# Kernel tuning notes

Hardware: AMD Instinct MI355X
Metric: run time of the kernel (lower is better)

## Reference

```python
import jax, jax.numpy as jnp
import numpy as np
from jax import lax

EPS = 1e-5

def setup_inputs() -> dict:
    key = jax.random.key(0)
    ks = jax.random.split(key, 8)
    B, D, H, W = 2, 96, 96, 96
    K, N, R = 4, 16, 6
    return {
        "x": jax.random.normal(ks[0], (B, D, H, W), jnp.float32),
        "x_proj_weight": jax.random.normal(ks[1], (K, R + 2 * N, D), jnp.float32) * 0.05,
        "dt_projs_weight": jax.random.normal(ks[2], (K, D, R), jnp.float32) * 0.05,
        "dt_projs_bias": jax.random.normal(ks[3], (K, D), jnp.float32) * 0.05,
        "A_logs": jax.random.uniform(ks[4], (K * D, N), jnp.float32, 0.0, 1.0),
        "Ds": jax.random.normal(ks[5], (K * D,), jnp.float32) * 0.1,
        "norm_weight": jnp.ones((D,), jnp.float32),
        "norm_bias": jnp.zeros((D,), jnp.float32),
    }

def _cross_scan(x):
    # x: [B,C,H,W] -> xs: [B,4,C,L]; dirs: row-major, col-major, and their flips
    B, C, H, W = x.shape
    x_hw = x.reshape(B, C, H * W)
    x_wh = jnp.swapaxes(x, 2, 3).reshape(B, C, H * W)
    return jnp.stack([x_hw, x_wh, x_hw[..., ::-1], x_wh[..., ::-1]], axis=1)

def _cross_merge(ys, H, W):
    # ys: [B,4,C,L] -> y: [B,C,L]
    B, K, C, L = ys.shape
    ys = ys[:, 0:2] + ys[:, 2:4][..., ::-1]
    y_wh = jnp.swapaxes(ys[:, 1].reshape(B, C, W, H), 2, 3).reshape(B, C, L)
    return ys[:, 0] + y_wh

def _forward(x, x_proj_weight, dt_projs_weight, dt_projs_bias, A_logs, Ds,
             norm_weight, norm_bias):
    B, D, H, W = x.shape
    L = H * W
    K, _, R = dt_projs_weight.shape
    N = A_logs.shape[1]

    xs = _cross_scan(x)                                        # [B,K,D,L]
    x_dbl = jnp.einsum('bkdl,kcd->bkcl', xs, x_proj_weight)    # [B,K,R+2N,L]
    dts, Bs, Cs = x_dbl[:, :, :R], x_dbl[:, :, R:R + N], x_dbl[:, :, R + N:]
    dts = jnp.einsum('bkrl,kdr->bkdl', dts, dt_projs_weight)   # [B,K,D,L]

    A = -jnp.exp(A_logs).reshape(K, D, N)                      # [K,D,N]
    delta = jax.nn.softplus(dts + dt_projs_bias[None, :, :, None])  # [B,K,D,L]

    # time-major for scan
    u_t = jnp.moveaxis(xs, 3, 0)       # [L,B,K,D]
    d_t = jnp.moveaxis(delta, 3, 0)    # [L,B,K,D]
    B_t = jnp.moveaxis(Bs, 3, 0)       # [L,B,K,N]
    C_t = jnp.moveaxis(Cs, 3, 0)       # [L,B,K,N]

    def step(h, inp):
        u, dlt, b, c = inp
        h = jnp.exp(dlt[..., None] * A) * h + (dlt * u)[..., None] * b[:, :, None, :]
        y = jnp.einsum('bkdn,bkn->bkd', h, c)
        return h, y

    h0 = jnp.zeros((B, K, D, N), xs.dtype)
    _, ys = lax.scan(step, h0, (u_t, d_t, B_t, C_t))           # ys: [L,B,K,D]
    ys = jnp.moveaxis(ys, 0, 3)                                # [B,K,D,L]
    ys = ys + Ds.reshape(1, K, D, 1) * xs                      # skip term

    y = _cross_merge(ys, H, W)                                 # [B,D,L]
    y = jnp.swapaxes(y, 1, 2)                                  # [B,L,D]
    # out_norm: LayerNorm over channel dim
    mu = y.mean(-1, keepdims=True)
    var = y.var(-1, keepdims=True)
    y = (y - mu) / jnp.sqrt(var + EPS) * norm_weight + norm_bias
    return y.reshape(B, H, W, D)

def reference(x, x_proj_weight, dt_projs_weight, dt_projs_bias, A_logs, Ds,
              norm_weight, norm_bias):
    return _forward(x, x_proj_weight, dt_projs_weight, dt_projs_bias,
                    A_logs, Ds, norm_weight, norm_bias)
```

## Files before the change

kernel.cpp:

```cpp
#include <hip/hip_runtime.h>
#include <hip/hip_bf16.h>
#include <hip/hip_fp16.h>


constexpr int Bn = 2, Kn = 4, Dn = 96, Hn = 96, Wn = 96, Ln = Hn * Wn;
constexpr int Nn = 16, Rn = 6;
constexpr int TLn = 36, CCn = 256, CLn = 36;

#define DI __device__ __forceinline__

typedef _Float16 half2v __attribute__((ext_vector_type(2)));

DI float bf2f(unsigned short u) { return __uint_as_float(((unsigned)u) << 16); }
DI bool probe_bf16(const void* nw) { return ((const unsigned*)nw)[0] == 0x3F803F80u; }
DI float ld_in(const void* p, long i, bool bf) {
  return bf ? bf2f(((const unsigned short*)p)[i]) : ((const float*)p)[i];
}
DI float fexp2(float x) {
#if __has_builtin(__builtin_amdgcn_exp2f)
  return __builtin_amdgcn_exp2f(x);
#else
  return exp2f(x);
#endif
}
DI float softplus_fast(float v) {
  return (v > 15.f) ? v : __logf(1.f + __expf(v));
}
DI float dot2acc(unsigned a, unsigned b, float c) {
#if __has_builtin(__builtin_amdgcn_fdot2)
  half2v av, bv;
  __builtin_memcpy(&av, &a, 4);
  __builtin_memcpy(&bv, &b, 4);
  return __builtin_amdgcn_fdot2(av, bv, c, false);
#else
  __half2 ah = *(__half2*)&a, bh = *(__half2*)&b;
  float2 af = __half22float2(ah), bf2_ = __half22float2(bh);
  return fmaf(af.y, bf2_.y, fmaf(af.x, bf2_.x, c));
#endif
}
DI float quad_reduce_add(float v) {
  int a = __builtin_amdgcn_mov_dpp(__float_as_int(v), 0xB1, 0xF, 0xF, true);
  v += __int_as_float(a);
  int b = __builtin_amdgcn_mov_dpp(__float_as_int(v), 0x4E, 0xF, 0xF, true);
  v += __int_as_float(b);
  return v;
}
constexpr float LOG2E = 1.44269504088896340736f;

__global__ __launch_bounds__(256) void k_prep(
    const void* __restrict__ x, const void* __restrict__ xpw,
    const void* __restrict__ dtw, const void* __restrict__ dtb,
    const void* __restrict__ Al, const void* __restrict__ Ds,
    const void* __restrict__ nw, const void* __restrict__ nb,
    float* __restrict__ xl, float* __restrict__ xlT,
    __half* __restrict__ wp_h, unsigned* __restrict__ wdt_p,
    float* __restrict__ bias_f, float* __restrict__ Al_f,
    float* __restrict__ dsum, float* __restrict__ nw_f, float* __restrict__ nb_f) {
  __shared__ float tile[96 * 49];
  bool bf = probe_bf16(nw);
  int h = blockIdx.x, wh = blockIdx.y, b = blockIdx.z;
  int w0 = wh * 48;
  int tid = threadIdx.x;
  int fi = ((blockIdx.z * gridDim.y + blockIdx.y) * gridDim.x + blockIdx.x) *
               256 + tid;
  int fgs = gridDim.x * gridDim.y * gridDim.z * 256;
  for (int i = fi; i < Kn * 4000; i += fgs) {
    int k = i / 4000, r = i - k * 4000;
    int c = r / 100, dd = r - c * 100;
    wp_h[i] = __float2half(
        (c < 38 && dd < 96) ? ld_in(xpw, (long)k * 38 * 96 + c * 96 + dd, bf)
                            : 0.f);
  }
  for (int i = fi; i < Kn * Dn; i += fgs) {
    __half2 h01 = __floats2half2_rn(ld_in(dtw, (long)i * 6 + 0, bf),
                                    ld_in(dtw, (long)i * 6 + 1, bf));
    __half2 h23 = __floats2half2_rn(ld_in(dtw, (long)i * 6 + 2, bf),
                                    ld_in(dtw, (long)i * 6 + 3, bf));
    __half2 h45 = __floats2half2_rn(ld_in(dtw, (long)i * 6 + 4, bf),
                                    ld_in(dtw, (long)i * 6 + 5, bf));
    wdt_p[i * 3 + 0] = *(unsigned*)&h01;
    wdt_p[i * 3 + 1] = *(unsigned*)&h23;
    wdt_p[i * 3 + 2] = *(unsigned*)&h45;
    bias_f[i] = ld_in(dtb, i, bf);
  }
  for (int i = fi; i < Kn * Dn * Nn; i += fgs)
    Al_f[i] = -__expf(ld_in(Al, i, bf)) * LOG2E;
  for (int i = fi; i < Dn; i += fgs) {
    dsum[i] = ld_in(Ds, i, bf) + ld_in(Ds, 96 + i, bf) +
              ld_in(Ds, 192 + i, bf) + ld_in(Ds, 288 + i, bf);
    nw_f[i] = ld_in(nw, i, bf);
    nb_f[i] = ld_in(nb, i, bf);
  }
  long srcbase = (long)b * Dn * Ln + (long)h * 96 + w0;
  for (int i = tid; i < 96 * 48; i += 256) {
    int d = i / 48, w = i - d * 48;
    tile[d * 49 + w] = ld_in(x, srcbase + (long)d * Ln + w, bf);
  }
  __syncthreads();
  float* xlb = xl + (size_t)b * Ln * 96;
  float* xTb = xlT + (size_t)b * Ln * 96;
  for (int i = tid; i < 48 * 96; i += 256) {
    int w = i / 96, d = i - w * 96;
    float v = tile[d * 49 + w];
    xlb[(size_t)(h * 96 + w0 + w) * 96 + d] = v;
    xTb[(size_t)((w0 + w) * 96 + h) * 96 + d] = v;
  }
}

__global__ __launch_bounds__(256) void k_proj(
    const float* __restrict__ xl, const float* __restrict__ xlT,
    const __half* __restrict__ wp_h, const unsigned* __restrict__ wdt_p,
    const float* __restrict__ bias_f, const float* __restrict__ Al_f,
    __half2* __restrict__ ddu, __half* __restrict__ BCh,
    float* __restrict__ PSg) {
  constexpr int TL = TLn;
  __shared__ __half xt[TL * 102];
  __shared__ __half wp[40 * 100];
  __shared__ __half xd2[TL * 40];
  __shared__ unsigned wdt_u[96 * 4];
  __shared__ float bias[96];
  int tile = blockIdx.x, k = blockIdx.y, b = blockIdx.z;
  int l0 = tile * TL;
  int tid = threadIdx.x;
  bool rev = (k & 2) != 0;

  {
    const uint4* wsrc = (const uint4*)(wp_h + (size_t)k * 4000);
    for (int i = tid; i < 500; i += 256) ((uint4*)wp)[i] = wsrc[i];
    const unsigned* dsrc = wdt_p + (size_t)k * 288;
    for (int i = tid; i < 288; i += 256) {
      int d = i / 3, r = i - d * 3;
      wdt_u[d * 4 + r] = dsrc[i];
    }
    if (tid < 96) bias[tid] = bias_f[k * 96 + tid];
  }
  {
    const float* xsrc = ((k & 1) ? xlT : xl) + (size_t)b * Ln * 96;
    for (int i = tid; i < TL * 24; i += 256) {
      int r = i / 24, q = i - r * 24;
      int g = rev ? (Ln - 1 - l0 - r) : (l0 + r);
      float4 v = *(const float4*)(xsrc + (size_t)g * 96 + q * 4);
      *(__half2*)(&xt[r * 102 + q * 4]) = __floats2half2_rn(v.x, v.y);
      *(__half2*)(&xt[r * 102 + q * 4 + 2]) = __floats2half2_rn(v.z, v.w);
    }
  }
  __syncthreads();

  {
    for (int it = tid; it < TL * 8; it += 256) {
      int j = it >> 3, cg = it & 7;
      int c0 = cg * 5;
      float acc[5] = {0.f, 0.f, 0.f, 0.f, 0.f};
      for (int dd = 0; dd < 96; dd += 4) {
        uint2 xa = *(const uint2*)&xt[j * 102 + dd];
#pragma unroll
        for (int i = 0; i < 5; ++i) {
          uint2 wv = *(const uint2*)&wp[(c0 + i) * 100 + dd];
          acc[i] = dot2acc(xa.x, wv.x, acc[i]);
          acc[i] = dot2acc(xa.y, wv.y, acc[i]);
        }
      }
#pragma unroll
      for (int i = 0; i < 5; ++i) xd2[j * 40 + c0 + i] = __float2half(acc[i]);
    }
  }
  __syncthreads();

  size_t bk = (size_t)b * 4 + k;
  {
    __half2* o = (__half2*)(BCh + (bk * (size_t)Ln + l0) * 32);
    for (int i = tid; i < TL * 16; i += 256) {
      int j = i >> 4, cp = i & 15;
      int c = cp * 2;
      int ng = c >> 3, idx = c & 7;
      int ch = (idx < 4) ? (6 + ng * 4 + idx) : (22 + ng * 4 + (idx - 4));
      o[i] = *(const __half2*)&xd2[j * 40 + ch];
    }
  }
  if (tid < 192) {
    int d = tid >> 1, hg = tid & 1;
    unsigned wv0 = wdt_u[d * 4], wv1 = wdt_u[d * 4 + 1], wv2 = wdt_u[d * 4 + 2];
    float bd = bias[d];
    float ac2[8];
    *(float4*)&ac2[0] = *(const float4*)&Al_f[(k * 96 + d) * 16 + hg * 8];
    *(float4*)&ac2[4] = *(const float4*)&Al_f[(k * 96 + d) * 16 + hg * 8 + 4];
    float spsum = 0.f;
    float S[8] = {0.f, 0.f, 0.f, 0.f, 0.f, 0.f, 0.f, 0.f};
    __half2* dcol = ddu + (bk * (size_t)Ln + l0) * 96 + d;
#pragma unroll 2
    for (int t = 0; t < TL; ++t) {
      uint2 xr01 = *(const uint2*)&xd2[t * 40];
      unsigned xr2 = *(const unsigned*)&xd2[t * 40 + 4];
      float v = dot2acc(xr01.x, wv0,
                dot2acc(xr01.y, wv1,
                dot2acc(xr2, wv2, bd)));
      float sp = softplus_fast(v);
      __half sph = __float2half(sp);
      float spc = __half2float(sph);
      float u = __half2float(xt[t * 102 + d]);
      __half fyh = __float2half(spc * u);
      float fy = __half2float(fyh);
      if (hg == 0) dcol[(size_t)t * 96] = __halves2half2(sph, fyh);
      spsum += spc;
      unsigned bw0 = *(const unsigned*)&xd2[t * 40 + 6 + hg * 8];
      unsigned bw1 = *(const unsigned*)&xd2[t * 40 + 8 + hg * 8];
      unsigned bw2 = *(const unsigned*)&xd2[t * 40 + 10 + hg * 8];
      unsigned bw3 = *(const unsigned*)&xd2[t * 40 + 12 + hg * 8];
      unsigned bws[4] = {bw0, bw1, bw2, bw3};
#pragma unroll
      for (int w = 0; w < 4; ++w) {
        float2 Bv = __half22float2(*(__half2*)&bws[w]);
        float a0 = fexp2(spc * ac2[w * 2]);
        S[w * 2] = fmaf(a0, S[w * 2], fy * Bv.x);
        float a1 = fexp2(spc * ac2[w * 2 + 1]);
        S[w * 2 + 1] = fmaf(a1, S[w * 2 + 1], fy * Bv.y);
      }
    }
    float P[8];
#pragma unroll
    for (int j = 0; j < 8; ++j) P[j] = fexp2(spsum * ac2[j]);
    size_t ob = ((size_t)(bk * 96 + d) * CCn + tile) * 32 + hg * 8;
    *(float4*)&PSg[ob] = make_float4(P[0], P[1], P[2], P[3]);
    *(float4*)&PSg[ob + 4] = make_float4(P[4], P[5], P[6], P[7]);
    *(float4*)&PSg[ob + 16] = make_float4(S[0], S[1], S[2], S[3]);
    *(float4*)&PSg[ob + 20] = make_float4(S[4], S[5], S[6], S[7]);
  }
}

__global__ __launch_bounds__(256) void k_midscan(float* __restrict__ PSg) {
  __shared__ float Pl[256], Sl[256];
  int bkd = blockIdx.x;
  int tid = threadIdx.x;
  int g = tid >> 4, n = tid & 15;
  constexpr int CPG = CCn / 16;
  size_t base = ((size_t)bkd * CCn + (size_t)g * CPG) * 32 + n;
  float Pr[CPG], Sr[CPG];
#pragma unroll
  for (int i = 0; i < CPG; ++i) {
    Pr[i] = PSg[base + (size_t)i * 32];
    Sr[i] = PSg[base + (size_t)i * 32 + 16];
  }
  float Pa = 1.f, Sa = 0.f;
#pragma unroll
  for (int i = 0; i < CPG; ++i) { Sa = fmaf(Pr[i], Sa, Sr[i]); Pa *= Pr[i]; }
  Pl[tid] = Pa;
  Sl[tid] = Sa;
  __syncthreads();
#pragma unroll
  for (int s = 1; s < 16; s <<= 1) {
    float Pp = 1.f, Sp = 0.f;
    if (g >= s) { Pp = Pl[(g - s) * 16 + n]; Sp = Sl[(g - s) * 16 + n]; }
    __syncthreads();
    if (g >= s) {
      Sl[tid] = fmaf(Pl[tid], Sp, Sl[tid]);
      Pl[tid] *= Pp;
    }
    __syncthreads();
  }
  float h = (g == 0) ? 0.f : Sl[(g - 1) * 16 + n];
#pragma unroll
  for (int i = 0; i < CPG; ++i) {
    PSg[base + (size_t)i * 32] = h;
    h = fmaf(Pr[i], h, Sr[i]);
  }
}

__global__ __launch_bounds__(192) void k_scan2(
    const __half2* __restrict__ ddu, const __half* __restrict__ BCh,
    const float* __restrict__ Al_f, const float* __restrict__ PSg,
    __half* __restrict__ ysH) {
  __shared__ __half2 dd_s[CLn * 96];
  __shared__ __half bc_s[CLn * 32];
  int chunk = blockIdx.x, k = blockIdx.y, b = blockIdx.z;
  int tid = threadIdx.x;
  int dp = tid >> 2, ng = tid & 3;
  int d0 = dp * 2, n0 = ng * 4;
  int bk = b * 4 + k;
  int t0 = chunk * CLn;
  float ac[2][4];
#pragma unroll
  for (int dd = 0; dd < 2; ++dd)
#pragma unroll
    for (int j = 0; j < 4; ++j)
      ac[dd][j] = Al_f[(k * 96 + d0 + dd) * 16 + n0 + j];
  {
    const uint4* dsrc = (const uint4*)(ddu + ((size_t)bk * Ln + t0) * 96);
    uint4* ddst = (uint4*)dd_s;
    for (int i = tid; i < CLn * 96 / 4; i += 192) ddst[i] = dsrc[i];
    const uint4* bsrc = (const uint4*)(BCh + ((size_t)bk * Ln + t0) * 32);
    uint4* bdst = (uint4*)bc_s;
    for (int i = tid; i < CLn * 32 * 2 / 16; i += 192) bdst[i] = bsrc[i];
  }
  float4 ha = *(const float4*)(PSg + ((size_t)(bk * 96 + d0) * CCn + chunk) * 32 + n0);
  float4 hb = *(const float4*)(PSg + ((size_t)(bk * 96 + d0 + 1) * CCn + chunk) * 32 + n0);
  float h[2][4] = {{ha.x, ha.y, ha.z, ha.w}, {hb.x, hb.y, hb.z, hb.w}};
  __syncthreads();

#pragma unroll 2
  for (int t = 0; t < CLn; ++t) {
    union { uint2 u; __half2 h2[2]; } dv;
    dv.u = *(const uint2*)&dd_s[t * 96 + d0];
    union { uint4 u; __half2 h2[4]; } bc;
    bc.u = *(const uint4*)&bc_s[t * 32 + ng * 8];
    float2 f0 = __half22float2(dv.h2[0]);
    float2 f1 = __half22float2(dv.h2[1]);
    float2 b01 = __half22float2(bc.h2[0]);
    float2 b23 = __half22float2(bc.h2[1]);
    float2 c01 = __half22float2(bc.h2[2]);
    float2 c23 = __half22float2(bc.h2[3]);
    float Ba[4] = {b01.x, b01.y, b23.x, b23.y};
    float Ca[4] = {c01.x, c01.y, c23.x, c23.y};
    float py0 = 0.f, py1 = 0.f;
#pragma unroll
    for (int j = 0; j < 4; ++j) {
      float a0 = fexp2(f0.x * ac[0][j]);
      h[0][j] = fmaf(a0, h[0][j], f0.y * Ba[j]);
      py0 = fmaf(h[0][j], Ca[j], py0);
      float a1 = fexp2(f1.x * ac[1][j]);
      h[1][j] = fmaf(a1, h[1][j], f1.y * Ba[j]);
      py1 = fmaf(h[1][j], Ca[j], py1);
    }
    py0 = quad_reduce_add(py0);
    py1 = quad_reduce_add(py1);
    if (ng == 0)
      *(__half2*)&ysH[((size_t)bk * Ln + t0 + t) * 96 + d0] =
          __halves2half2(__float2half(py0), __float2half(py1));
  }
}

__global__ __launch_bounds__(256) void k_merge_ln(
    const __half* __restrict__ ysH, const float* __restrict__ xl,
    const float* __restrict__ dsum, const void* __restrict__ nwraw,
    const float* __restrict__ nw_f, const float* __restrict__ nb_f,
    void* __restrict__ outv) {
  __shared__ float yt[32 * 98];
  __shared__ float nwf[96], nbf[96], dsm[96], mu_s[32], rs_s[32];
  bool bf = probe_bf16(nwraw);
  int tile = blockIdx.x, b = blockIdx.y;
  int h0 = (tile / 12) * 4, w0 = (tile % 12) * 8;
  int tid = threadIdx.x;
  if (tid < 96) {
    nwf[tid] = nw_f[tid];
    nbf[tid] = nb_f[tid];
    dsm[tid] = dsum[tid];
  }
  const __half* y0 = ysH + (size_t)(b * 4 + 0) * Ln * 96;
  const __half* y1 = ysH + (size_t)(b * 4 + 1) * Ln * 96;
  const __half* y2 = ysH + (size_t)(b * 4 + 2) * Ln * 96;
  const __half* y3 = ysH + (size_t)(b * 4 + 3) * Ln * 96;
  const float* xb = xl + (size_t)b * Ln * 96;
  __syncthreads();
  for (int i = tid; i < 32 * 48; i += 256) {
    int rr = i / 48, dp = i - rr * 48, d = dp * 2;
    int hh = h0 + (rr >> 3), ww = w0 + (rr & 7);
    int l = hh * 96 + ww, t1 = ww * 96 + hh;
    float2 v0 = __half22float2(*(const __half2*)&y0[(size_t)l * 96 + d]);
    float2 v1 = __half22float2(*(const __half2*)&y1[(size_t)t1 * 96 + d]);
    float2 v2 = __half22float2(*(const __half2*)&y2[(size_t)(Ln - 1 - l) * 96 + d]);
    float2 v3 = __half22float2(*(const __half2*)&y3[(size_t)(Ln - 1 - t1) * 96 + d]);
    float2 xv = *(const float2*)&xb[(size_t)l * 96 + d];
    float2 r;
    r.x = v0.x + v1.x + v2.x + v3.x + dsm[d] * xv.x;
    r.y = v0.y + v1.y + v2.y + v3.y + dsm[d + 1] * xv.y;
    *(float2*)&yt[rr * 98 + d] = r;
  }
  __syncthreads();
  {
    int rr = tid >> 3, qq = tid & 7;
    float s = 0.f, ss = 0.f;
#pragma unroll 4
    for (int j = 0; j < 12; ++j) {
      float v = yt[rr * 98 + qq * 12 + j];
      s += v;
      ss += v * v;
    }
#pragma unroll
    for (int m = 1; m < 8; m <<= 1) {
      s += __shfl_xor(s, m, 64);
      ss += __shfl_xor(ss, m, 64);
    }
    if (qq == 0) {
      float mu = s * (1.f / 96.f);
      float var = fmaxf(ss * (1.f / 96.f) - mu * mu, 0.f);
      mu_s[rr] = mu;
      rs_s[rr] = rsqrtf(var + 1e-5f);
    }
  }
  __syncthreads();
  for (int i = tid; i < 32 * 48; i += 256) {
    int rr = i / 48, dp = i - rr * 48, d = dp * 2;
    int hh = h0 + (rr >> 3), ww = w0 + (rr & 7);
    size_t idx = ((size_t)b * Ln + hh * 96 + ww) * 96 + d;
    float2 yv = *(const float2*)&yt[rr * 98 + d];
    float mu = mu_s[rr], rs = rs_s[rr];
    float o0 = (yv.x - mu) * rs * nwf[d] + nbf[d];
    float o1 = (yv.y - mu) * rs * nwf[d + 1] + nbf[d + 1];
    if (bf) {
      union { unsigned u; unsigned short us[2]; } pk;
      __hip_bfloat16 b0 = __float2bfloat16(o0), b1 = __float2bfloat16(o1);
      pk.us[0] = *(unsigned short*)&b0;
      pk.us[1] = *(unsigned short*)&b1;
      *(unsigned*)&((__hip_bfloat16*)outv)[idx] = pk.u;
    } else {
      *(float2*)&((float*)outv)[idx] = make_float2(o0, o1);
    }
  }
}

extern "C" void kernel_launch(void* const* d_in, const int* in_sizes, int n_in,
                              void* d_out, int out_size, void* d_ws, size_t ws_size,
                              hipStream_t stream) {
  const void* x   = d_in[0];
  const void* xpw = d_in[1];
  const void* dtw = d_in[2];
  const void* dtb = d_in[3];
  const void* Al  = d_in[4];
  const void* Ds  = d_in[5];
  const void* nw  = d_in[6];
  const void* nb  = d_in[7];

  char* ws = (char*)d_ws;
  size_t off = 0;
  auto alloc = [&](size_t bytes) {
    char* p = ws + off;
    off += (bytes + 511) & ~(size_t)511;
    return p;
  };
  float* xl    = (float*)alloc((size_t)Bn * Ln * Dn * 4);
  float* xlT   = (float*)alloc((size_t)Bn * Ln * Dn * 4);
  __half* wp_h = (__half*)alloc((size_t)Kn * 4000 * 2);
  unsigned* wdt_p = (unsigned*)alloc((size_t)Kn * Dn * 3 * 4);
  float* bias_f= (float*)alloc((size_t)Kn * Dn * 4);
  float* Al_f  = (float*)alloc((size_t)Kn * Dn * Nn * 4);
  float* dsum  = (float*)alloc((size_t)Dn * 4);
  float* nw_f  = (float*)alloc((size_t)Dn * 4);
  float* nb_f  = (float*)alloc((size_t)Dn * 4);
  __half2* ddu = (__half2*)alloc((size_t)Bn * Kn * Ln * Dn * 4);
  __half* BCh  = (__half*)alloc((size_t)Bn * Kn * Ln * 32 * 2);
  float* PS    = (float*)alloc((size_t)Bn * Kn * Dn * CCn * 32 * 4);
  __half* ysH  = (__half*)alloc((size_t)Bn * Kn * Ln * Dn * 2);
  (void)ws_size; (void)in_sizes; (void)n_in; (void)out_size;

  k_prep<<<dim3(Hn, 2, Bn), dim3(256), 0, stream>>>(
      x, xpw, dtw, dtb, Al, Ds, nw, nb, xl, xlT, wp_h, wdt_p, bias_f, Al_f,
      dsum, nw_f, nb_f);
  k_proj<<<dim3(Ln / TLn, Kn, Bn), dim3(256), 0, stream>>>(
      xl, xlT, wp_h, wdt_p, bias_f, Al_f, ddu, BCh, PS);
  k_midscan<<<dim3(Bn * Kn * Dn), dim3(256), 0, stream>>>(PS);
  k_scan2<<<dim3(CCn, Kn, Bn), dim3(192), 0, stream>>>(ddu, BCh, Al_f, PS, ysH);
  k_merge_ln<<<dim3(288, Bn), dim3(256), 0, stream>>>(ysH, xl, dsum, nw, nw_f,
                                                      nb_f, d_out);
}
```

Before: 205.6 us.

## Shrink scan chunk to 32, pad dt weights, accumulate chunk decay products inline

Changes the scan chunk length from 36 to 32 (288 chunks) so that k_proj's projection maps one row per lane with no remainder loop. It also pads the dt-projection weights to 4 words per channel so they load as uint4. The per-chunk decay product is now accumulated multiplicatively from the per-step exponentials, which are already computed, instead of being recomputed from a running softplus sum. The extra chunk count makes k_midscan serialize more work per group (CPG=18) and enlarges the PS buffer. The chunk-boundary P values may also round slightly differently.

New measurement: 176.4 us. 14.2% less time.

```diff
diff --git a/kernel.cpp b/kernel.cpp
--- a/kernel.cpp
+++ b/kernel.cpp
@@ -5,7 +5,7 @@
 
 constexpr int Bn = 2, Kn = 4, Dn = 96, Hn = 96, Wn = 96, Ln = Hn * Wn;
 constexpr int Nn = 16, Rn = 6;
-constexpr int TLn = 36, CCn = 256, CLn = 36;
+constexpr int CCn = 288, CLn = 32;
 
 #define DI __device__ __forceinline__
 
@@ -78,9 +78,10 @@
                                     ld_in(dtw, (long)i * 6 + 3, bf));
     __half2 h45 = __floats2half2_rn(ld_in(dtw, (long)i * 6 + 4, bf),
                                     ld_in(dtw, (long)i * 6 + 5, bf));
-    wdt_p[i * 3 + 0] = *(unsigned*)&h01;
-    wdt_p[i * 3 + 1] = *(unsigned*)&h23;
-    wdt_p[i * 3 + 2] = *(unsigned*)&h45;
+    wdt_p[i * 4 + 0] = *(unsigned*)&h01;
+    wdt_p[i * 4 + 1] = *(unsigned*)&h23;
+    wdt_p[i * 4 + 2] = *(unsigned*)&h45;
+    wdt_p[i * 4 + 3] = 0u;
     bias_f[i] = ld_in(dtb, i, bf);
   }
   for (int i = fi; i < Kn * Dn * Nn; i += fgs)
@@ -113,7 +114,7 @@
     const float* __restrict__ bias_f, const float* __restrict__ Al_f,
     __half2* __restrict__ ddu, __half* __restrict__ BCh,
     float* __restrict__ PSg) {
-  constexpr int TL = TLn;
+  constexpr int TL = 32;
   __shared__ __half xt[TL * 102];
   __shared__ __half wp[40 * 100];
   __shared__ __half xd2[TL * 40];
@@ -127,11 +128,8 @@
   {
     const uint4* wsrc = (const uint4*)(wp_h + (size_t)k * 4000);
     for (int i = tid; i < 500; i += 256) ((uint4*)wp)[i] = wsrc[i];
-    const unsigned* dsrc = wdt_p + (size_t)k * 288;
-    for (int i = tid; i < 288; i += 256) {
-      int d = i / 3, r = i - d * 3;
-      wdt_u[d * 4 + r] = dsrc[i];
-    }
+    const uint4* dsrc = (const uint4*)(wdt_p + (size_t)k * 384);
+    for (int i = tid; i < 96; i += 256) ((uint4*)wdt_u)[i] = dsrc[i];
     if (tid < 96) bias[tid] = bias_f[k * 96 + tid];
   }
   {
@@ -147,22 +145,20 @@
   __syncthreads();
 
   {
-    for (int it = tid; it < TL * 8; it += 256) {
-      int j = it >> 3, cg = it & 7;
-      int c0 = cg * 5;
-      float acc[5] = {0.f, 0.f, 0.f, 0.f, 0.f};
-      for (int dd = 0; dd < 96; dd += 4) {
-        uint2 xa = *(const uint2*)&xt[j * 102 + dd];
-#pragma unroll
-        for (int i = 0; i < 5; ++i) {
-          uint2 wv = *(const uint2*)&wp[(c0 + i) * 100 + dd];
-          acc[i] = dot2acc(xa.x, wv.x, acc[i]);
-          acc[i] = dot2acc(xa.y, wv.y, acc[i]);
-        }
+    int jg = tid & 31, cg = tid >> 5;
+    int c0 = cg * 5;
+    float acc[5] = {0.f, 0.f, 0.f, 0.f, 0.f};
+    for (int dd = 0; dd < 96; dd += 4) {
+      uint2 xa = *(const uint2*)&xt[jg * 102 + dd];
+#pragma unroll
+      for (int i = 0; i < 5; ++i) {
+        uint2 wv = *(const uint2*)&wp[(c0 + i) * 100 + dd];
+        acc[i] = dot2acc(xa.x, wv.x, acc[i]);
+        acc[i] = dot2acc(xa.y, wv.y, acc[i]);
       }
-#pragma unroll
-      for (int i = 0; i < 5; ++i) xd2[j * 40 + c0 + i] = __float2half(acc[i]);
-    }
+    }
+#pragma unroll
+    for (int i = 0; i < 5; ++i) xd2[jg * 40 + c0 + i] = __float2half(acc[i]);
   }
   __syncthreads();
 
@@ -184,7 +180,7 @@
     float ac2[8];
     *(float4*)&ac2[0] = *(const float4*)&Al_f[(k * 96 + d) * 16 + hg * 8];
     *(float4*)&ac2[4] = *(const float4*)&Al_f[(k * 96 + d) * 16 + hg * 8 + 4];
-    float spsum = 0.f;
+    float P[8] = {1.f, 1.f, 1.f, 1.f, 1.f, 1.f, 1.f, 1.f};
     float S[8] = {0.f, 0.f, 0.f, 0.f, 0.f, 0.f, 0.f, 0.f};
     __half2* dcol = ddu + (bk * (size_t)Ln + l0) * 96 + d;
 #pragma unroll 2
@@ -195,30 +191,23 @@
                 dot2acc(xr01.y, wv1,
                 dot2acc(xr2, wv2, bd)));
       float sp = softplus_fast(v);
-      __half sph = __float2half(sp);
-      float spc = __half2float(sph);
       float u = __half2float(xt[t * 102 + d]);
-      __half fyh = __float2half(spc * u);
-      float fy = __half2float(fyh);
-      if (hg == 0) dcol[(size_t)t * 96] = __halves2half2(sph, fyh);
-      spsum += spc;
-      unsigned bw0 = *(const unsigned*)&xd2[t * 40 + 6 + hg * 8];
-      unsigned bw1 = *(const unsigned*)&xd2[t * 40 + 8 + hg * 8];
-      unsigned bw2 = *(const unsigned*)&xd2[t * 40 + 10 + hg * 8];
-      unsigned bw3 = *(const unsigned*)&xd2[t * 40 + 12 + hg * 8];
-      unsigned bws[4] = {bw0, bw1, bw2, bw3};
+      __half2 pk = __floats2half2_rn(sp, sp * u);
+      if (hg == 0) dcol[(size_t)t * 96] = pk;
+      float2 pf = __half22float2(pk);
+      float spc = pf.x, fy = pf.y;
 #pragma unroll
       for (int w = 0; w < 4; ++w) {
-        float2 Bv = __half22float2(*(__half2*)&bws[w]);
+        unsigned bw = *(const unsigned*)&xd2[t * 40 + 6 + 8 * hg + 2 * w];
+        float2 Bv = __half22float2(*(__half2*)&bw);
         float a0 = fexp2(spc * ac2[w * 2]);
+        P[w * 2] *= a0;
         S[w * 2] = fmaf(a0, S[w * 2], fy * Bv.x);
         float a1 = fexp2(spc * ac2[w * 2 + 1]);
+        P[w * 2 + 1] *= a1;
         S[w * 2 + 1] = fmaf(a1, S[w * 2 + 1], fy * Bv.y);
       }
     }
-    float P[8];
-#pragma unroll
-    for (int j = 0; j < 8; ++j) P[j] = fexp2(spsum * ac2[j]);
     size_t ob = ((size_t)(bk * 96 + d) * CCn + tile) * 32 + hg * 8;
     *(float4*)&PSg[ob] = make_float4(P[0], P[1], P[2], P[3]);
     *(float4*)&PSg[ob + 4] = make_float4(P[4], P[5], P[6], P[7]);
@@ -429,7 +418,7 @@
   float* xl    = (float*)alloc((size_t)Bn * Ln * Dn * 4);
   float* xlT   = (float*)alloc((size_t)Bn * Ln * Dn * 4);
   __half* wp_h = (__half*)alloc((size_t)Kn * 4000 * 2);
-  unsigned* wdt_p = (unsigned*)alloc((size_t)Kn * Dn * 3 * 4);
+  unsigned* wdt_p = (unsigned*)alloc((size_t)Kn * Dn * 4 * 4);
   float* bias_f= (float*)alloc((size_t)Kn * Dn * 4);
   float* Al_f  = (float*)alloc((size_t)Kn * Dn * Nn * 4);
   float* dsum  = (float*)alloc((size_t)Dn * 4);
@@ -444,7 +433,7 @@
   k_prep<<<dim3(Hn, 2, Bn), dim3(256), 0, stream>>>(
       x, xpw, dtw, dtb, Al, Ds, nw, nb, xl, xlT, wp_h, wdt_p, bias_f, Al_f,
       dsum, nw_f, nb_f);
-  k_proj<<<dim3(Ln / TLn, Kn, Bn), dim3(256), 0, stream>>>(
+  k_proj<<<dim3(Ln / 32, Kn, Bn), dim3(256), 0, stream>>>(
       xl, xlT, wp_h, wdt_p, bias_f, Al_f, ddu, BCh, PS);
   k_midscan<<<dim3(Bn * Kn * Dn), dim3(256), 0, stream>>>(PS);
   k_scan2<<<dim3(CCn, Kn, Bn), dim3(192), 0, stream>>>(ddu, BCh, Al_f, PS, ysH);
```
